# Kernel optimization log

Hardware: AMD Instinct MI355X
Metric: run time of the kernel (lower is better)

## Reference

```python
import jax, jax.numpy as jnp
import numpy as np

EPS = 1e-5

def mlp_layer(h, W, b, g, be):
    # Linear -> BatchNorm1d (training-mode batch stats over points) -> LeakyReLU
    y = h @ W + b
    mu = jnp.mean(y, axis=0)
    var = jnp.mean((y - mu) ** 2, axis=0)
    y = (y - mu) * jax.lax.rsqrt(var + EPS) * g + be
    return jax.nn.leaky_relu(y, 0.01)

def segment_unit_norm(pos, idx, S):
    # center each segment on its centroid, scale to the unit sphere, return radius*2 as diameter
    N = pos.shape[0]
    cnt = jax.ops.segment_sum(jnp.ones((N,), pos.dtype), idx, num_segments=S)
    center = jax.ops.segment_sum(pos, idx, num_segments=S) / jnp.maximum(cnt, 1.0)[:, None]
    centered = pos - center[idx]
    r2 = jax.ops.segment_max(jnp.sum(centered * centered, axis=1), idx, num_segments=S)
    r = jnp.sqrt(jnp.maximum(r2, 0.0))  # empty segments -> -inf clamped to 0
    r_safe = jnp.where(r > 0.0, r, 1.0)
    pos_n = centered / r_safe[idx][:, None]
    diameter = 2.0 * r_safe * (cnt > 0).astype(pos.dtype)
    return pos_n, diameter, cnt

def segment_max_pool(x, idx, S, cnt):
    out = jax.ops.segment_max(x, idx, num_segments=S)
    return jnp.where((cnt > 0)[:, None], out, 0.0)

def setup_inputs() -> dict:
    key = jax.random.key(0)
    ks = jax.random.split(key, 16)
    N, S = 1000000, 10000
    Cx = 64
    loc = [Cx + 3, 128, 256]
    glo = [loc[-1] + 1, 512, 512]
    d = {
        'pos': jax.random.normal(ks[0], (N, 3), jnp.float32),
        'x': jax.random.normal(ks[1], (N, Cx), jnp.float32),
        'idx': jnp.sort(jax.random.randint(ks[2], (N,), 0, S)),
        'num_segments': S,
    }
    def lin(k, fan_in, fan_out):
        s = 1.0 / np.sqrt(fan_in)
        return jax.random.uniform(k, (fan_in, fan_out), jnp.float32, -s, s)
    # local MLP params
    d['W1'], d['b1'] = lin(ks[3], loc[0], loc[1]), jnp.zeros((loc[1],), jnp.float32)
    d['g1'], d['be1'] = jnp.ones((loc[1],), jnp.float32), jnp.zeros((loc[1],), jnp.float32)
    d['W2'], d['b2'] = lin(ks[4], loc[1], loc[2]), jnp.zeros((loc[2],), jnp.float32)
    d['g2'], d['be2'] = jnp.ones((loc[2],), jnp.float32), jnp.zeros((loc[2],), jnp.float32)
    # global MLP params
    d['GW1'], d['Gb1'] = lin(ks[5], glo[0], glo[1]), jnp.zeros((glo[1],), jnp.float32)
    d['Gg1'], d['Gbe1'] = jnp.ones((glo[1],), jnp.float32), jnp.zeros((glo[1],), jnp.float32)
    d['GW2'], d['Gb2'] = lin(ks[6], glo[1], glo[2]), jnp.zeros((glo[2],), jnp.float32)
    d['Gg2'], d['Gbe2'] = jnp.ones((glo[2],), jnp.float32), jnp.zeros((glo[2],), jnp.float32)
    return d

def reference(pos, x, idx, num_segments, W1, b1, g1, be1, W2, b2, g2, be2, GW1, Gb1, Gg1, Gbe1, GW2, Gb2, Gg2, Gbe2):
    S = num_segments
    pos_n, diameter, cnt = segment_unit_norm(pos, idx, S)
    h = jnp.concatenate([x, pos_n], axis=1)            # [N, 67]
    h = mlp_layer(h, W1, b1, g1, be1)                   # [N, 128]
    h = mlp_layer(h, W2, b2, g2, be2)                   # [N, 256]
    hg = segment_max_pool(h, idx, S, cnt)               # [S, 256]
    hg = jnp.concatenate([hg, diameter[:, None]], axis=1)  # [S, 257]
    hg = mlp_layer(hg, GW1, Gb1, Gg1, Gbe1)             # [S, 512]
    hg = mlp_layer(hg, GW2, Gb2, Gg2, Gbe2)             # [S, 512]
    return hg
```

## Files before the change

kernel.cpp:

```cpp
#include <hip/hip_runtime.h>
#include <hip/hip_fp16.h>

#define LEAKY(v) ((v) < 0.0f ? 0.01f * (v) : (v))

typedef _Float16 half8 __attribute__((ext_vector_type(8)));
typedef float f32x4 __attribute__((ext_vector_type(4)));

__device__ __forceinline__ unsigned int pkrtz(float a, float b) {
  auto h = __builtin_amdgcn_cvt_pkrtz(a, b);
  union { decltype(h) h2; unsigned int u; } c; c.h2 = h; return c.u;
}
__device__ __forceinline__ unsigned short f2h(float f) {
  union { _Float16 h; unsigned short u; } c; c.h = (_Float16)f; return c.u;
}
__device__ __forceinline__ unsigned int fkey(float f) {
  unsigned int u = __float_as_uint(f);
  return ((int)u < 0) ? ~u : (u | 0x80000000u);
}
__device__ __forceinline__ float fdec(unsigned int k) {
  return __uint_as_float((k & 0x80000000u) ? (k ^ 0x80000000u) : ~k);
}


__global__ void seg_lb_kernel(const int* __restrict__ idx, int N, int S, int* __restrict__ seg_start) {
  int s = blockIdx.x * blockDim.x + threadIdx.x;
  if (s > S) return;
  int lo = 0, hi = N;
  while (lo < hi) {
    int mid = (lo + hi) >> 1;
    if (idx[mid] < s) lo = mid + 1; else hi = mid;
  }
  seg_start[s] = lo;
}

__global__ void seg_stat_kernel(const float* __restrict__ pos, const int* __restrict__ seg_start,
                                float* __restrict__ center, float* __restrict__ invr,
                                float* __restrict__ diam) {
  int s = blockIdx.x;
  int start = seg_start[s], end = seg_start[s + 1];
  int cnt = end - start;
  int lane = threadIdx.x;
  float sx = 0.f, sy = 0.f, sz = 0.f;
  for (int i = start + lane; i < end; i += 64) {
    sx += pos[3 * i + 0]; sy += pos[3 * i + 1]; sz += pos[3 * i + 2];
  }
  for (int o = 32; o > 0; o >>= 1) {
    sx += __shfl_down(sx, o); sy += __shfl_down(sy, o); sz += __shfl_down(sz, o);
  }
  float inv_cnt = 1.0f / fmaxf((float)cnt, 1.0f);
  float cx = __shfl(sx, 0) * inv_cnt;
  float cy = __shfl(sy, 0) * inv_cnt;
  float cz = __shfl(sz, 0) * inv_cnt;
  float m2 = 0.f;
  for (int i = start + lane; i < end; i += 64) {
    float dx = pos[3 * i + 0] - cx, dy = pos[3 * i + 1] - cy, dz = pos[3 * i + 2] - cz;
    m2 = fmaxf(m2, dx * dx + dy * dy + dz * dz);
  }
  for (int o = 32; o > 0; o >>= 1) m2 = fmaxf(m2, __shfl_down(m2, o));
  if (lane == 0) {
    float r = sqrtf(fmaxf(m2, 0.f));
    float rs = (r > 0.f) ? r : 1.0f;
    center[3 * s + 0] = cx; center[3 * s + 1] = cy; center[3 * s + 2] = cz;
    invr[s] = 1.0f / rs;
    diam[s] = (cnt > 0) ? 2.0f * rs : 0.0f;
  }
}


__global__ void wconv_kernel(const float* __restrict__ W, int K, int N, unsigned short* __restrict__ Wt) {
  int i = blockIdx.x * 256 + threadIdx.x;
  if (i >= N * 16) return;
  int n = i >> 4, c = i & 15;
  union { uint4 u; unsigned short h[8]; } o;
#pragma unroll
  for (int e = 0; e < 8; ++e) {
    int k = c * 8 + e;
    float v = (k < K) ? W[(size_t)k * N + n] : 0.f;
    o.h[e] = f2h(v);
  }
  *(uint4*)&Wt[(size_t)n * 128 + c * 8] = o.u;
}


__global__ __launch_bounds__(256, 2) void gemm1_kernel(
    const float* __restrict__ x, const float* __restrict__ pos, const int* __restrict__ idx,
    const float* __restrict__ center, const float* __restrict__ invr,
    const unsigned short* __restrict__ w1t, const float* __restrict__ b1,
    unsigned short* __restrict__ y1, float* __restrict__ gsum, float* __restrict__ gsq,
    int M, int ntiles) {
  __shared__ __align__(16) unsigned short Asm[128 * 128];
  __shared__ __align__(16) unsigned short Osm[128 * 128];
  const int tid = threadIdx.x;
  const int och = tid & 15;
  const int rr = tid >> 4;
  const int lane = tid & 63;
  const int wv = tid >> 6;
  const int wr = wv >> 1, wc = wv & 1;
  const int lr = lane & 15, lg = lane >> 4;
  const int tstep = gridDim.x;

  half8 b[4][3];
#pragma unroll
  for (int cf = 0; cf < 4; ++cf) {
    int n = wc * 64 + cf * 16 + lr;
#pragma unroll
    for (int ks = 0; ks < 3; ++ks) {
      int c = ks * 4 + lg;
      b[cf][ks] = *(const half8*)&w1t[n * 128 + c * 8];
    }
  }
  float bb[4];
#pragma unroll
  for (int cf = 0; cf < 4; ++cf) bb[cf] = b1[wc * 64 + cf * 16 + lr];

  if (tid < 128) {
    uint4 z = make_uint4(0u, 0u, 0u, 0u);
    int r = tid;
    *(uint4*)&Asm[r * 128 + ((9 ^ (r & 7)) << 3)] = z;
    *(uint4*)&Asm[r * 128 + ((10 ^ (r & 7)) << 3)] = z;
    *(uint4*)&Asm[r * 128 + ((11 ^ (r & 7)) << 3)] = z;
  }

  float4 pfx[8];
  float pp0 = 0.f, pp1 = 0.f, pp2 = 0.f, pc0 = 0.f, pc1 = 0.f, pc2 = 0.f, pir = 0.f;

  auto prefetch = [&](int tt) {
#pragma unroll
    for (int j = 0; j < 4; ++j) {
      int c = tid + 256 * j;
      int r = c >> 3, cc = c & 7;
      int row = tt * 128 + r;
      pfx[2 * j] = make_float4(0.f, 0.f, 0.f, 0.f);
      pfx[2 * j + 1] = make_float4(0.f, 0.f, 0.f, 0.f);
      if (row < M) {
        pfx[2 * j]     = *(const float4*)&x[(size_t)row * 64 + cc * 8];
        pfx[2 * j + 1] = *(const float4*)&x[(size_t)row * 64 + cc * 8 + 4];
      }
    }
    if (tid < 128) {
      int row = tt * 128 + tid;
      pp0 = pp1 = pp2 = pc0 = pc1 = pc2 = 0.f; pir = 0.f;
      if (row < M) {
        int s = idx[row];
        pp0 = pos[3 * row + 0]; pp1 = pos[3 * row + 1]; pp2 = pos[3 * row + 2];
        pc0 = center[3 * s + 0]; pc1 = center[3 * s + 1]; pc2 = center[3 * s + 2];
        pir = invr[s];
      }
    }
  };
  auto stageA = [&]() {
#pragma unroll
    for (int j = 0; j < 4; ++j) {
      int c = tid + 256 * j;
      int r = c >> 3, cc = c & 7;
      uint4 o;
      o.x = pkrtz(pfx[2 * j].x, pfx[2 * j].y);
      o.y = pkrtz(pfx[2 * j].z, pfx[2 * j].w);
      o.z = pkrtz(pfx[2 * j + 1].x, pfx[2 * j + 1].y);
      o.w = pkrtz(pfx[2 * j + 1].z, pfx[2 * j + 1].w);
      *(uint4*)&Asm[r * 128 + ((cc ^ (r & 7)) << 3)] = o;
    }
    if (tid < 128) {
      int r = tid;
      uint4 o = make_uint4(0u, 0u, 0u, 0u);
      o.x = pkrtz((pp0 - pc0) * pir, (pp1 - pc1) * pir);
      o.y = pkrtz((pp2 - pc2) * pir, 0.f);
      *(uint4*)&Asm[r * 128 + ((8 ^ (r & 7)) << 3)] = o;
    }
  };

  int t = blockIdx.x;
  prefetch(t);
  stageA();
  __syncthreads();

  float psum[8], psq[8];
#pragma unroll
  for (int c = 0; c < 8; ++c) { psum[c] = 0.f; psq[c] = 0.f; }

  const f32x4 fzero = {0.f, 0.f, 0.f, 0.f};

  for (;;) {
    const int tn = t + tstep;
    const bool more = tn < ntiles;
    if (more) prefetch(tn);
    f32x4 acc[4][4];
#pragma unroll
    for (int rf = 0; rf < 4; ++rf)
#pragma unroll
      for (int cf = 0; cf < 4; ++cf) acc[rf][cf] = fzero;
#pragma unroll
    for (int ks = 0; ks < 3; ++ks) {
      half8 a[4];
      int c = ks * 4 + lg;
#pragma unroll
      for (int rf = 0; rf < 4; ++rf) {
        int row = wr * 64 + rf * 16 + lr;
        a[rf] = *(const half8*)&Asm[row * 128 + ((c ^ (row & 7)) << 3)];
      }
#pragma unroll
      for (int cf = 0; cf < 4; ++cf)
#pragma unroll
        for (int rf = 0; rf < 4; ++rf)
          acc[rf][cf] = __builtin_amdgcn_mfma_f32_16x16x32_f16(a[rf], b[cf][ks], acc[rf][cf], 0, 0, 0);
    }
#pragma unroll
    for (int cf = 0; cf < 4; ++cf) {
      int col = wc * 64 + cf * 16 + lr;
#pragma unroll
      for (int rf = 0; rf < 4; ++rf) {
#pragma unroll
        for (int r = 0; r < 4; ++r) {
          int row = wr * 64 + rf * 16 + lg * 4 + r;
          Osm[row * 128 + (((col >> 3) ^ (row & 7)) << 3) + (col & 7)] = f2h(acc[rf][cf][r] + bb[cf]);
        }
      }
    }
    __syncthreads();
    const int row0 = t * 128;
#pragma unroll
    for (int j = 0; j < 8; ++j) {
      int r = rr + 16 * j;
      int row = row0 + r;
      if (row < M) {
        uint4 v = *(const uint4*)&Osm[r * 128 + ((och ^ (r & 7)) << 3)];
        *(uint4*)&y1[(size_t)row * 128 + och * 8] = v;
        union { uint4 u; _Float16 h[8]; } w; w.u = v;
#pragma unroll
        for (int c = 0; c < 8; ++c) { float f = (float)w.h[c]; psum[c] += f; psq[c] += f * f; }
      }
    }
    if (!more) break;
    stageA();
    t = tn;
    __syncthreads();
  }

  __syncthreads();
  float* redS = (float*)Osm;
  float* redQ = redS + 16 * 128;
#pragma unroll
  for (int c = 0; c < 8; ++c) {
    redS[rr * 128 + och * 8 + c] = psum[c];
    redQ[rr * 128 + och * 8 + c] = psq[c];
  }
  __syncthreads();
  if (tid < 128) {
    float s = 0.f, q = 0.f;
#pragma unroll
    for (int g = 0; g < 16; ++g) { s += redS[g * 128 + tid]; q += redQ[g * 128 + tid]; }
    atomicAdd(&gsum[tid], s);
    atomicAdd(&gsq[tid], q);
  }
}


__global__ __launch_bounds__(256, 2) void gemm2_kernel(
    const unsigned short* __restrict__ y1,
    const unsigned short* __restrict__ a1h, const unsigned short* __restrict__ c1h,
    const unsigned short* __restrict__ w2t, const float* __restrict__ b2,
    const int* __restrict__ idx,
    unsigned int* __restrict__ segmx, unsigned int* __restrict__ segmn,
    float* __restrict__ gsum, float* __restrict__ gsq,
    int M, int ntiles) {
  __shared__ __align__(16) unsigned short Asm[128 * 128];
  __shared__ __align__(16) unsigned short Osm[128 * 128];
  __shared__ int sbuf[2][128];
  const int tid = threadIdx.x;
  const int col0 = blockIdx.x * 128;
  const int och = tid & 15;
  const int rr = tid >> 4;
  const int tstep = gridDim.y;

  const _Float16* ap = (const _Float16*)a1h;
  const _Float16* cp = (const _Float16*)c1h;
  _Float16 av[8], cv[8];
#pragma unroll
  for (int q = 0; q < 8; ++q) { av[q] = ap[och * 8 + q]; cv[q] = cp[och * 8 + q]; }

#pragma unroll
  for (int j = 0; j < 8; ++j) {
    int n = rr + 16 * j;
    uint4 v = *(const uint4*)&w2t[(size_t)(col0 + n) * 128 + och * 8];
    *(uint4*)&Osm[n * 128 + ((och ^ (n & 7)) << 3)] = v;
  }

  int t = blockIdx.y;
  uint4 pf[8];
#pragma unroll
  for (int j = 0; j < 8; ++j) {
    int row = t * 128 + rr + 16 * j;
    pf[j] = make_uint4(0u, 0u, 0u, 0u);
    if (row < M) pf[j] = *(const uint4*)&y1[(size_t)row * 128 + och * 8];
  }
  if (tid < 128) {
    int row = t * 128 + tid;
    sbuf[0][tid] = (row < M) ? idx[row] : -1;
  }
  __syncthreads();

  const int lane = tid & 63;
  const int wv = tid >> 6;
  const int wr = wv >> 1, wc = wv & 1;
  const int lr = lane & 15, lg = lane >> 4;

  half8 b[4][4];
#pragma unroll
  for (int cf = 0; cf < 4; ++cf) {
    int n = wc * 64 + cf * 16 + lr;
#pragma unroll
    for (int ks = 0; ks < 4; ++ks) {
      int c = ks * 4 + lg;
      b[cf][ks] = *(const half8*)&Osm[n * 128 + ((c ^ (n & 7)) << 3)];
    }
  }
  float bb[4];
#pragma unroll
  for (int cf = 0; cf < 4; ++cf) bb[cf] = b2[col0 + wc * 64 + cf * 16 + lr];

#pragma unroll
  for (int j = 0; j < 8; ++j) {
    int r = rr + 16 * j;
    union { uint4 u; _Float16 h[8]; } w; w.u = pf[j];
#pragma unroll
    for (int q = 0; q < 8; ++q) {
      _Float16 v = w.h[q] * av[q] + cv[q];
      w.h[q] = (v < (_Float16)0.f) ? v * (_Float16)0.01f : v;
    }
    *(uint4*)&Asm[r * 128 + ((och ^ (r & 7)) << 3)] = w.u;
  }
  __syncthreads();

  const int scol = tid & 127;
  const int sh = tid >> 7;
  float psumc = 0.f, psqc = 0.f;
  int p = 0;

  const f32x4 fzero = {0.f, 0.f, 0.f, 0.f};

  for (;;) {
    const int tn = t + tstep;
    const bool more = tn < ntiles;
    if (more) {
#pragma unroll
      for (int j = 0; j < 8; ++j) {
        int row = tn * 128 + rr + 16 * j;
        pf[j] = make_uint4(0u, 0u, 0u, 0u);
        if (row < M) pf[j] = *(const uint4*)&y1[(size_t)row * 128 + och * 8];
      }
      if (tid < 128) {
        int row = tn * 128 + tid;
        sbuf[p ^ 1][tid] = (row < M) ? idx[row] : -1;
      }
    }
    f32x4 acc[4][4];
#pragma unroll
    for (int rf = 0; rf < 4; ++rf)
#pragma unroll
      for (int cf = 0; cf < 4; ++cf) acc[rf][cf] = fzero;
#pragma unroll
    for (int ks = 0; ks < 4; ++ks) {
      half8 a[4];
      int c = ks * 4 + lg;
#pragma unroll
      for (int rf = 0; rf < 4; ++rf) {
        int row = wr * 64 + rf * 16 + lr;
        a[rf] = *(const half8*)&Asm[row * 128 + ((c ^ (row & 7)) << 3)];
      }
#pragma unroll
      for (int cf = 0; cf < 4; ++cf)
#pragma unroll
        for (int rf = 0; rf < 4; ++rf)
          acc[rf][cf] = __builtin_amdgcn_mfma_f32_16x16x32_f16(a[rf], b[cf][ks], acc[rf][cf], 0, 0, 0);
    }
#pragma unroll
    for (int cf = 0; cf < 4; ++cf) {
      int col = wc * 64 + cf * 16 + lr;
#pragma unroll
      for (int rf = 0; rf < 4; ++rf) {
#pragma unroll
        for (int r = 0; r < 4; ++r) {
          int row = wr * 64 + rf * 16 + lg * 4 + r;
          Osm[row * 128 + (((col >> 3) ^ (row & 7)) << 3) + (col & 7)] = f2h(acc[rf][cf][r] + bb[cf]);
        }
      }
    }
    __syncthreads();
    {
      int rows = M - t * 128; if (rows > 128) rows = 128;
      int rbeg = sh * 64;
      int rend = rbeg + 64; if (rend > rows) rend = rows;
      float mx = -3.4e38f, mn = 3.4e38f;
      const int* sids = sbuf[p];
      int cur = (rbeg < rend) ? sids[rbeg] : -1;
      for (int r = rbeg; r < rend; ++r) {
        int sgm = sids[r];
        float v = (float)*(const _Float16*)&Osm[r * 128 + (((scol >> 3) ^ (r & 7)) << 3) + (scol & 7)];
        if (sgm != cur) {
          atomicMax(&segmx[(size_t)cur * 256 + col0 + scol], fkey(mx));
          atomicMin(&segmn[(size_t)cur * 256 + col0 + scol], fkey(mn));
          mx = -3.4e38f; mn = 3.4e38f; cur = sgm;
        }
        mx = fmaxf(mx, v); mn = fminf(mn, v);
        psumc += v; psqc += v * v;
      }
      if (cur >= 0) {
        atomicMax(&segmx[(size_t)cur * 256 + col0 + scol], fkey(mx));
        atomicMin(&segmn[(size_t)cur * 256 + col0 + scol], fkey(mn));
      }
    }
    if (!more) break;
#pragma unroll
    for (int j = 0; j < 8; ++j) {
      int r = rr + 16 * j;
      union { uint4 u; _Float16 h[8]; } w; w.u = pf[j];
#pragma unroll
      for (int q = 0; q < 8; ++q) {
        _Float16 v = w.h[q] * av[q] + cv[q];
        w.h[q] = (v < (_Float16)0.f) ? v * (_Float16)0.01f : v;
      }
      *(uint4*)&Asm[r * 128 + ((och ^ (r & 7)) << 3)] = w.u;
    }
    t = tn; p ^= 1;
    __syncthreads();
  }

  __syncthreads();
  float* red = (float*)Asm;
  if (sh) { red[scol] = psumc; red[128 + scol] = psqc; }
  __syncthreads();
  if (!sh) {
    atomicAdd(&gsum[col0 + scol], psumc + red[scol]);
    atomicAdd(&gsq[col0 + scol], psqc + red[128 + scol]);
  }
}


__device__ __forceinline__ void mm_tile(const float* __restrict__ As, const float* __restrict__ Bs,
                                        int bk, int tr, int tc, float acc[4][8]) {
  for (int k4 = 0; k4 < bk; k4 += 4) {
    float4 a[4];
#pragma unroll
    for (int r = 0; r < 4; ++r) a[r] = *(const float4*)&As[(tr * 4 + r) * 68 + k4];
#pragma unroll
    for (int kk = 0; kk < 4; ++kk) {
      float4 w0 = *(const float4*)&Bs[(k4 + kk) * 128 + tc * 8];
      float4 w1 = *(const float4*)&Bs[(k4 + kk) * 128 + tc * 8 + 4];
#pragma unroll
      for (int r = 0; r < 4; ++r) {
        float av = (kk == 0) ? a[r].x : (kk == 1) ? a[r].y : (kk == 2) ? a[r].z : a[r].w;
        acc[r][0] = fmaf(av, w0.x, acc[r][0]);
        acc[r][1] = fmaf(av, w0.y, acc[r][1]);
        acc[r][2] = fmaf(av, w0.z, acc[r][2]);
        acc[r][3] = fmaf(av, w0.w, acc[r][3]);
        acc[r][4] = fmaf(av, w1.x, acc[r][4]);
        acc[r][5] = fmaf(av, w1.y, acc[r][5]);
        acc[r][6] = fmaf(av, w1.z, acc[r][6]);
        acc[r][7] = fmaf(av, w1.w, acc[r][7]);
      }
    }
  }
}

__device__ __forceinline__ void stats_reduce(float* redS, float* redQ,
                                             const float psum[8], const float psq[8],
                                             int tr, int tc, int tid,
                                             float* __restrict__ gsum, float* __restrict__ gsq, int col0) {
  __syncthreads();
#pragma unroll
  for (int c = 0; c < 8; ++c) {
    redS[tr * 128 + tc * 8 + c] = psum[c];
    redQ[tr * 128 + tc * 8 + c] = psq[c];
  }
  __syncthreads();
  if (tid < 128) {
    float s = 0.f, q = 0.f;
#pragma unroll
    for (int r = 0; r < 16; ++r) { s += redS[r * 128 + tid]; q += redQ[r * 128 + tid]; }
    atomicAdd(&gsum[col0 + tid], s);
    atomicAdd(&gsq[col0 + tid], q);
  }
}


template <bool NORM>
__global__ __launch_bounds__(256) void gemmG_kernel(
    const float* __restrict__ A, int lda, int K, int M,
    const float* __restrict__ an, const float* __restrict__ cn,
    const float* __restrict__ W, const float* __restrict__ bias,
    float* __restrict__ Y, float* __restrict__ gsum, float* __restrict__ gsq) {
  __shared__ float As[64 * 68];
  __shared__ float Bs[64 * 128];
  const int tid = threadIdx.x;
  const int row0 = blockIdx.x * 64;
  const int col0 = blockIdx.y * 128;
  const int tr = tid >> 4, tc = tid & 15;
  float acc[4][8];
#pragma unroll
  for (int r = 0; r < 4; ++r)
#pragma unroll
    for (int c = 0; c < 8; ++c) acc[r][c] = 0.f;

  const int nkb = (K + 63) >> 6;
  for (int kb = 0; kb < nkb; ++kb) {
    if (kb) __syncthreads();
    for (int e = tid; e < 64 * 64; e += 256) {
      int r = e >> 6, c = e & 63;
      int row = row0 + r, k = kb * 64 + c;
      float v = 0.f;
      if (row < M && k < K) {
        v = A[(size_t)row * lda + k];
        if (NORM) { v = an[k] * v + cn[k]; v = LEAKY(v); }
      }
      As[r * 68 + c] = v;
    }
    for (int e = tid; e < 64 * 32; e += 256) {
      int r = e >> 5, c4 = e & 31;
      int k = kb * 64 + r;
      float4 v = make_float4(0.f, 0.f, 0.f, 0.f);
      if (k < K) v = *(const float4*)&W[(size_t)k * 512 + col0 + c4 * 4];
      *(float4*)&Bs[r * 128 + c4 * 4] = v;
    }
    __syncthreads();
    mm_tile(As, Bs, 64, tr, tc, acc);
  }

  float psum[8], psq[8];
#pragma unroll
  for (int c = 0; c < 8; ++c) { psum[c] = 0.f; psq[c] = 0.f; }
#pragma unroll
  for (int r = 0; r < 4; ++r) {
    int row = row0 + tr * 4 + r;
    if (row < M) {
      float yv[8];
#pragma unroll
      for (int c = 0; c < 8; ++c) {
        yv[c] = acc[r][c] + bias[col0 + tc * 8 + c];
        psum[c] += yv[c]; psq[c] += yv[c] * yv[c];
      }
      *(float4*)&Y[(size_t)row * 512 + col0 + tc * 8] = make_float4(yv[0], yv[1], yv[2], yv[3]);
      *(float4*)&Y[(size_t)row * 512 + col0 + tc * 8 + 4] = make_float4(yv[4], yv[5], yv[6], yv[7]);
    }
  }
  stats_reduce(As, Bs, psum, psq, tr, tc, tid, gsum, gsq, col0);
}


__global__ void finalize_kernel(const float* __restrict__ gsum, const float* __restrict__ gsq,
                                const float* __restrict__ g, const float* __restrict__ be,
                                float invn, int C, float* __restrict__ a, float* __restrict__ c,
                                unsigned short* __restrict__ ah, unsigned short* __restrict__ chh) {
  int j = blockIdx.x * blockDim.x + threadIdx.x;
  if (j >= C) return;
  float mu = gsum[j] * invn;
  float var = gsq[j] * invn - mu * mu;
  float aj = g[j] * rsqrtf(var + 1e-5f);
  float cj = be[j] - mu * aj;
  a[j] = aj;
  c[j] = cj;
  if (ah) { ah[j] = f2h(aj); chh[j] = f2h(cj); }
}


__global__ void poolfin_kernel(const unsigned int* __restrict__ segmx, const unsigned int* __restrict__ segmn,
                               const int* __restrict__ seg_start,
                               const float* __restrict__ a2, const float* __restrict__ c2,
                               const float* __restrict__ diam, float* __restrict__ hg) {
  int s = blockIdx.x;
  int j = threadIdx.x;
  bool nonempty = seg_start[s + 1] > seg_start[s];
  float aj = a2[j], cj = c2[j];
  unsigned int k = (aj >= 0.f) ? segmx[(size_t)s * 256 + j] : segmn[(size_t)s * 256 + j];
  float f = fdec(k);
  float v = aj * f + cj;
  v = LEAKY(v);
  hg[(size_t)s * 257 + j] = nonempty ? v : 0.0f;
  if (j == 0) hg[(size_t)s * 257 + 256] = diam[s];
}


__global__ void final_kernel(const float* __restrict__ y4, const float* __restrict__ a4,
                             const float* __restrict__ c4, float* __restrict__ out, int total) {
  int i = blockIdx.x * blockDim.x + threadIdx.x;
  if (i >= total) return;
  int j = i & 511;
  float v = a4[j] * y4[i] + c4[j];
  out[i] = LEAKY(v);
}


extern "C" void kernel_launch(void* const* d_in, const int* in_sizes, int n_in,
                              void* d_out, int out_size, void* d_ws, size_t ws_size,
                              hipStream_t stream) {
  const float* pos  = (const float*)d_in[0];
  const float* x    = (const float*)d_in[1];
  const int*   idx  = (const int*)d_in[2];
  const float* W1   = (const float*)d_in[4];
  const float* b1   = (const float*)d_in[5];
  const float* g1   = (const float*)d_in[6];
  const float* be1  = (const float*)d_in[7];
  const float* W2   = (const float*)d_in[8];
  const float* b2   = (const float*)d_in[9];
  const float* g2   = (const float*)d_in[10];
  const float* be2  = (const float*)d_in[11];
  const float* GW1  = (const float*)d_in[12];
  const float* Gb1  = (const float*)d_in[13];
  const float* Gg1  = (const float*)d_in[14];
  const float* Gbe1 = (const float*)d_in[15];
  const float* GW2  = (const float*)d_in[16];
  const float* Gb2  = (const float*)d_in[17];
  const float* Gg2  = (const float*)d_in[18];
  const float* Gbe2 = (const float*)d_in[19];
  float* out = (float*)d_out;

  const int N = in_sizes[0] / 3;
  const int S = 10000;

  char* ws = (char*)d_ws;
  size_t off = 0;
  auto take = [&](size_t bytes) -> char* {
    char* p = ws + off;
    off = (off + bytes + 255) & ~(size_t)255;
    return p;
  };
  int*   seg_start = (int*)take((size_t)(S + 1) * sizeof(int));
  float* center    = (float*)take((size_t)S * 3 * sizeof(float));
  float* invr      = (float*)take((size_t)S * sizeof(float));
  float* diam      = (float*)take((size_t)S * sizeof(float));
  float* stats     = (float*)take(2816 * sizeof(float));
  float* gsum1 = stats,        *gsq1 = stats + 128;
  float* gsum2 = stats + 256,  *gsq2 = stats + 512;
  float* gsum3 = stats + 768,  *gsq3 = stats + 1280;
  float* gsum4 = stats + 1792, *gsq4 = stats + 2304;
  float* par = (float*)take(2816 * sizeof(float));
  float* a1 = par,        *c1 = par + 256;
  float* a2 = par + 512,  *c2 = par + 768;
  float* a3 = par + 1024, *c3 = par + 1536;
  float* a4 = par + 2048, *c4 = par + 2560;
  unsigned short* a1h = (unsigned short*)take(128 * 2);
  unsigned short* c1h = (unsigned short*)take(128 * 2);
  unsigned short* w1t = (unsigned short*)take((size_t)128 * 128 * 2);
  unsigned short* w2t = (unsigned short*)take((size_t)256 * 128 * 2);
  float* hg = (float*)take((size_t)S * 257 * sizeof(float));
  float* y3 = (float*)take((size_t)S * 512 * sizeof(float));
  float* y4 = (float*)take((size_t)S * 512 * sizeof(float));
  unsigned int* segmx = (unsigned int*)take((size_t)S * 256 * sizeof(unsigned int));
  unsigned int* segmn = (unsigned int*)take((size_t)S * 256 * sizeof(unsigned int));
  unsigned short* y1 = (unsigned short*)take((size_t)N * 128 * 2);
  (void)ws_size; (void)n_in; (void)out_size;

  hipMemsetAsync(stats, 0, 2816 * sizeof(float), stream);
  hipMemsetAsync(segmx, 0x00, (size_t)S * 256 * sizeof(unsigned int), stream);
  hipMemsetAsync(segmn, 0xFF, (size_t)S * 256 * sizeof(unsigned int), stream);

  wconv_kernel<<<(128 * 16 + 255) / 256, 256, 0, stream>>>(W1, 67, 128, w1t);
  wconv_kernel<<<(256 * 16 + 255) / 256, 256, 0, stream>>>(W2, 128, 256, w2t);

  seg_lb_kernel<<<(S + 1 + 255) / 256, 256, 0, stream>>>(idx, N, S, seg_start);
  seg_stat_kernel<<<S, 64, 0, stream>>>(pos, seg_start, center, invr, diam);

  const int ntiles = (N + 127) / 128;
  gemm1_kernel<<<512, 256, 0, stream>>>(x, pos, idx, center, invr, w1t, b1, y1, gsum1, gsq1, N, ntiles);
  finalize_kernel<<<1, 128, 0, stream>>>(gsum1, gsq1, g1, be1, 1.0f / (float)N, 128, a1, c1, a1h, c1h);

  gemm2_kernel<<<dim3(2, 256), 256, 0, stream>>>(y1, a1h, c1h, w2t, b2, idx, segmx, segmn,
                                                 gsum2, gsq2, N, ntiles);
  finalize_kernel<<<1, 256, 0, stream>>>(gsum2, gsq2, g2, be2, 1.0f / (float)N, 256, a2, c2, nullptr, nullptr);

  poolfin_kernel<<<S, 256, 0, stream>>>(segmx, segmn, seg_start, a2, c2, diam, hg);

  gemmG_kernel<false><<<dim3((S + 63) / 64, 4), 256, 0, stream>>>(hg, 257, 257, S, nullptr, nullptr,
                                                                  GW1, Gb1, y3, gsum3, gsq3);
  finalize_kernel<<<2, 256, 0, stream>>>(gsum3, gsq3, Gg1, Gbe1, 1.0f / (float)S, 512, a3, c3, nullptr, nullptr);

  gemmG_kernel<true><<<dim3((S + 63) / 64, 4), 256, 0, stream>>>(y3, 512, 512, S, a3, c3,
                                                                 GW2, Gb2, y4, gsum4, gsq4);
  finalize_kernel<<<2, 256, 0, stream>>>(gsum4, gsq4, Gg2, Gbe2, 1.0f / (float)S, 512, a4, c4, nullptr, nullptr);

  final_kernel<<<(S * 512 + 255) / 256, 256, 0, stream>>>(y4, a4, c4, out, S * 512);
}
```

Measured before the change: 708.9 us.

## Reduce segment max/min and BN stats directly from MFMA registers with permuted rows

Loads each 128-row tile of y1 in a permuted row order so that every lane's MFMA accumulator fragment covers 16 consecutive original rows. Segment max/min atomics and the per-column sum/sumsq partials are then computed straight from registers, with no fp16 round-trip through an output LDS tile. The freed LDS becomes a double buffer for the A tile, which removes the per-tile store-then-sync of outputs, and the final stats use wave shuffles. The trade-off is more atomics per tile: one set per 16-row run per lane instead of per 64-row run per thread. Statistics are now taken in fp32 rather than fp16-rounded values.

```diff
diff --git a/kernel.cpp b/kernel.cpp
--- a/kernel.cpp
+++ b/kernel.cpp
@@ -263,8 +263,7 @@
     unsigned int* __restrict__ segmx, unsigned int* __restrict__ segmn,
     float* __restrict__ gsum, float* __restrict__ gsq,
     int M, int ntiles) {
-  __shared__ __align__(16) unsigned short Asm[128 * 128];
-  __shared__ __align__(16) unsigned short Osm[128 * 128];
+  __shared__ __align__(16) unsigned short Abuf[2][128 * 128];
   __shared__ int sbuf[2][128];
   const int tid = threadIdx.x;
   const int col0 = blockIdx.x * 128;
@@ -278,24 +277,26 @@
 #pragma unroll
   for (int q = 0; q < 8; ++q) { av[q] = ap[och * 8 + q]; cv[q] = cp[och * 8 + q]; }
 
+  int t = blockIdx.y;
+  uint4 pf[8];
+  auto perm = [](int p) { return (p & 0x43) | ((p & 0x30) >> 2) | ((p & 0x0c) << 2); };
+#pragma unroll
+  for (int j = 0; j < 8; ++j) {
+    int r = rr + 16 * j;
+    int row = t * 128 + perm(r);
+    pf[j] = make_uint4(0u, 0u, 0u, 0u);
+    if (row < M) pf[j] = *(const uint4*)&y1[(size_t)row * 128 + och * 8];
+  }
+  if (tid < 128) {
+    int row = t * 128 + tid;
+    sbuf[0][tid] = (row < M) ? idx[row] : -1;
+  }
+
 #pragma unroll
   for (int j = 0; j < 8; ++j) {
     int n = rr + 16 * j;
     uint4 v = *(const uint4*)&w2t[(size_t)(col0 + n) * 128 + och * 8];
-    *(uint4*)&Osm[n * 128 + ((och ^ (n & 7)) << 3)] = v;
-  }
-
-  int t = blockIdx.y;
-  uint4 pf[8];
-#pragma unroll
-  for (int j = 0; j < 8; ++j) {
-    int row = t * 128 + rr + 16 * j;
-    pf[j] = make_uint4(0u, 0u, 0u, 0u);
-    if (row < M) pf[j] = *(const uint4*)&y1[(size_t)row * 128 + och * 8];
-  }
-  if (tid < 128) {
-    int row = t * 128 + tid;
-    sbuf[0][tid] = (row < M) ? idx[row] : -1;
+    *(uint4*)&Abuf[0][n * 128 + ((och ^ (n & 7)) << 3)] = v;
   }
   __syncthreads();
 
@@ -311,12 +312,13 @@
 #pragma unroll
     for (int ks = 0; ks < 4; ++ks) {
       int c = ks * 4 + lg;
-      b[cf][ks] = *(const half8*)&Osm[n * 128 + ((c ^ (n & 7)) << 3)];
+      b[cf][ks] = *(const half8*)&Abuf[0][n * 128 + ((c ^ (n & 7)) << 3)];
     }
   }
   float bb[4];
 #pragma unroll
   for (int cf = 0; cf < 4; ++cf) bb[cf] = b2[col0 + wc * 64 + cf * 16 + lr];
+  __syncthreads();
 
 #pragma unroll
   for (int j = 0; j < 8; ++j) {
@@ -327,16 +329,16 @@
       _Float16 v = w.h[q] * av[q] + cv[q];
       w.h[q] = (v < (_Float16)0.f) ? v * (_Float16)0.01f : v;
     }
-    *(uint4*)&Asm[r * 128 + ((och ^ (r & 7)) << 3)] = w.u;
-  }
-  __syncthreads();
-
-  const int scol = tid & 127;
-  const int sh = tid >> 7;
-  float psumc = 0.f, psqc = 0.f;
+    *(uint4*)&Abuf[0][r * 128 + ((och ^ (r & 7)) << 3)] = w.u;
+  }
+  __syncthreads();
+
+  float csum[4], csq[4];
+#pragma unroll
+  for (int cf = 0; cf < 4; ++cf) { csum[cf] = 0.f; csq[cf] = 0.f; }
+
+  const f32x4 fzero = {0.f, 0.f, 0.f, 0.f};
   int p = 0;
-
-  const f32x4 fzero = {0.f, 0.f, 0.f, 0.f};
 
   for (;;) {
     const int tn = t + tstep;
@@ -344,7 +346,8 @@
     if (more) {
 #pragma unroll
       for (int j = 0; j < 8; ++j) {
-        int row = tn * 128 + rr + 16 * j;
+        int r = rr + 16 * j;
+        int row = tn * 128 + perm(r);
         pf[j] = make_uint4(0u, 0u, 0u, 0u);
         if (row < M) pf[j] = *(const uint4*)&y1[(size_t)row * 128 + och * 8];
       }
@@ -358,6 +361,7 @@
     for (int rf = 0; rf < 4; ++rf)
 #pragma unroll
       for (int cf = 0; cf < 4; ++cf) acc[rf][cf] = fzero;
+    const unsigned short* Ac = Abuf[p];
 #pragma unroll
     for (int ks = 0; ks < 4; ++ks) {
       half8 a[4];
@@ -365,7 +369,7 @@
 #pragma unroll
       for (int rf = 0; rf < 4; ++rf) {
         int row = wr * 64 + rf * 16 + lr;
-        a[rf] = *(const half8*)&Asm[row * 128 + ((c ^ (row & 7)) << 3)];
+        a[rf] = *(const half8*)&Ac[row * 128 + ((c ^ (row & 7)) << 3)];
       }
 #pragma unroll
       for (int cf = 0; cf < 4; ++cf)
@@ -373,40 +377,45 @@
         for (int rf = 0; rf < 4; ++rf)
           acc[rf][cf] = __builtin_amdgcn_mfma_f32_16x16x32_f16(a[rf], b[cf][ks], acc[rf][cf], 0, 0, 0);
     }
-#pragma unroll
-    for (int cf = 0; cf < 4; ++cf) {
-      int col = wc * 64 + cf * 16 + lr;
-#pragma unroll
-      for (int rf = 0; rf < 4; ++rf) {
-#pragma unroll
-        for (int r = 0; r < 4; ++r) {
-          int row = wr * 64 + rf * 16 + lg * 4 + r;
-          Osm[row * 128 + (((col >> 3) ^ (row & 7)) << 3) + (col & 7)] = f2h(acc[rf][cf][r] + bb[cf]);
+    {
+      const int* sp = &sbuf[p][wr * 64 + lg * 16];
+      int4 s0 = *(const int4*)&sp[0];
+      int4 s1 = *(const int4*)&sp[4];
+      int4 s2 = *(const int4*)&sp[8];
+      int4 s3 = *(const int4*)&sp[12];
+      int sid[16] = { s0.x, s0.y, s0.z, s0.w, s1.x, s1.y, s1.z, s1.w,
+                      s2.x, s2.y, s2.z, s2.w, s3.x, s3.y, s3.z, s3.w };
+#pragma unroll
+      for (int cf = 0; cf < 4; ++cf) {
+        const unsigned col = col0 + wc * 64 + cf * 16 + lr;
+        float vv[16];
+#pragma unroll
+        for (int rf = 0; rf < 4; ++rf)
+#pragma unroll
+          for (int r = 0; r < 4; ++r) vv[rf * 4 + r] = acc[rf][cf][r] + bb[cf];
+#pragma unroll
+        for (int k = 0; k < 16; ++k) {
+          float vk = (sid[k] >= 0) ? vv[k] : 0.f;
+          csum[cf] += vk; csq[cf] += vk * vk;
         }
-      }
-    }
-    __syncthreads();
-    {
-      int rows = M - t * 128; if (rows > 128) rows = 128;
-      int rbeg = sh * 64;
-      int rend = rbeg + 64; if (rend > rows) rend = rows;
-      float mx = -3.4e38f, mn = 3.4e38f;
-      const int* sids = sbuf[p];
-      int cur = (rbeg < rend) ? sids[rbeg] : -1;
-      for (int r = rbeg; r < rend; ++r) {
-        int sgm = sids[r];
-        float v = (float)*(const _Float16*)&Osm[r * 128 + (((scol >> 3) ^ (r & 7)) << 3) + (scol & 7)];
-        if (sgm != cur) {
-          atomicMax(&segmx[(size_t)cur * 256 + col0 + scol], fkey(mx));
-          atomicMin(&segmn[(size_t)cur * 256 + col0 + scol], fkey(mn));
-          mx = -3.4e38f; mn = 3.4e38f; cur = sgm;
+        int cur = sid[0];
+        float mx = vv[0], mn = vv[0];
+#pragma unroll
+        for (int k = 1; k < 16; ++k) {
+          if (sid[k] != cur) {
+            if (cur >= 0) {
+              atomicMax(&segmx[(size_t)cur * 256 + col], fkey(mx));
+              atomicMin(&segmn[(size_t)cur * 256 + col], fkey(mn));
+            }
+            cur = sid[k]; mx = vv[k]; mn = vv[k];
+          } else {
+            mx = fmaxf(mx, vv[k]); mn = fminf(mn, vv[k]);
+          }
         }
-        mx = fmaxf(mx, v); mn = fminf(mn, v);
-        psumc += v; psqc += v * v;
-      }
-      if (cur >= 0) {
-        atomicMax(&segmx[(size_t)cur * 256 + col0 + scol], fkey(mx));
-        atomicMin(&segmn[(size_t)cur * 256 + col0 + scol], fkey(mn));
+        if (cur >= 0) {
+          atomicMax(&segmx[(size_t)cur * 256 + col], fkey(mx));
+          atomicMin(&segmn[(size_t)cur * 256 + col], fkey(mn));
+        }
       }
     }
     if (!more) break;
@@ -419,19 +428,26 @@
         _Float16 v = w.h[q] * av[q] + cv[q];
         w.h[q] = (v < (_Float16)0.f) ? v * (_Float16)0.01f : v;
       }
-      *(uint4*)&Asm[r * 128 + ((och ^ (r & 7)) << 3)] = w.u;
+      *(uint4*)&Abuf[p ^ 1][r * 128 + ((och ^ (r & 7)) << 3)] = w.u;
     }
     t = tn; p ^= 1;
     __syncthreads();
   }
 
-  __syncthreads();
-  float* red = (float*)Asm;
-  if (sh) { red[scol] = psumc; red[128 + scol] = psqc; }
-  __syncthreads();
-  if (!sh) {
-    atomicAdd(&gsum[col0 + scol], psumc + red[scol]);
-    atomicAdd(&gsq[col0 + scol], psqc + red[128 + scol]);
+#pragma unroll
+  for (int cf = 0; cf < 4; ++cf) {
+    csum[cf] += __shfl_xor(csum[cf], 16);
+    csum[cf] += __shfl_xor(csum[cf], 32);
+    csq[cf] += __shfl_xor(csq[cf], 16);
+    csq[cf] += __shfl_xor(csq[cf], 32);
+  }
+  if (lg == 0) {
+#pragma unroll
+    for (int cf = 0; cf < 4; ++cf) {
+      int col = col0 + wc * 64 + cf * 16 + lr;
+      atomicAdd(&gsum[col], csum[cf]);
+      atomicAdd(&gsq[col], csq[cf]);
+    }
   }
 }
 
```

Result: faster. 690.2 us, median of 3 (-2.6%).
